# Optimization experiments

Measured on AMD Instinct MI355X. Metric: run time of the kernel, lower is better.

Reference implementation:

```python
import jax, jax.numpy as jnp
import numpy as np

E, T, H, I, K = 16, 2048, 1024, 512, 2  # experts, tokens, hidden, intermediate, top_k


def setup_inputs() -> dict:
    key = jax.random.key(0)
    k1, k2, k3, k4, k5 = jax.random.split(key, 5)
    hidden_states = jax.random.normal(k1, (T, H), dtype=jnp.float32)
    topk_weights = jax.random.uniform(k2, (T, K), dtype=jnp.float32)
    topk_indices = jax.random.randint(k3, (T, K), 0, E, dtype=jnp.int32)
    # learned expert params, viewed per expert as in _view_experts_weight()
    gate_up_proj = jax.random.normal(k4, (E, H, 2 * I), dtype=jnp.float32) * 0.02
    down_proj = jax.random.normal(k5, (E, I, H), dtype=jnp.float32) * 0.02
    return {
        "hidden_states": hidden_states,
        "topk_weights": topk_weights,
        "topk_indices": topk_indices,
        "gate_up_proj": gate_up_proj,
        "down_proj": down_proj,
    }


def reference(hidden_states, topk_weights, topk_indices, gate_up_proj, down_proj):
    """MoE experts: per-expert gate_up GEMM -> silu-gate -> down GEMM,
    combined with top-k routing weights (index_add over tokens in the original).

    Equivalent dense formulation: combine[e, t] = sum_k topk_weights[t, k] * [topk_indices[t, k] == e];
    out = sum_e expert_e(hidden_states) * combine[e][:, None]. Tokens not routed to e get
    weight 0, matching the original gather/scatter-add exactly (including duplicate
    expert ids within a token, which accumulate).
    """
    num_experts = gate_up_proj.shape[0]
    one_hot = jax.nn.one_hot(topk_indices, num_experts, dtype=topk_weights.dtype)  # [T, K, E]
    combine = jnp.einsum("tk,tke->et", topk_weights, one_hot)  # [E, T]

    def body(acc, xs):
        w_gu, w_d, w = xs  # [H, 2I], [I, H], [T]
        gate_up = hidden_states @ w_gu  # [T, 2I]
        gate, up = jnp.split(gate_up, 2, axis=-1)
        expert_out = (jax.nn.silu(gate) * up) @ w_d  # [T, H]
        return acc + expert_out * w[:, None], None

    init = jnp.zeros_like(hidden_states)
    out, _ = jax.lax.scan(body, init, (gate_up_proj, down_proj, combine))
    return out.astype(hidden_states.dtype)
```

## Files before the change

### kernel.cpp

```cpp
#include <hip/hip_runtime.h>

#define E_ 16
#define T_ 2048
#define H_ 1024
#define I_ 512
#define K_ 2
#define NPAIR (T_*K_)

typedef __bf16 bf16x8 __attribute__((ext_vector_type(8)));
typedef float  f32x4  __attribute__((ext_vector_type(4)));

static __device__ __forceinline__ unsigned short f2bf(float f) {
    __bf16 h = (__bf16)f;
    return __builtin_bit_cast(unsigned short, h);
}

__global__ __launch_bounds__(256) void route_kernel(
    const float* __restrict__ tw, const int* __restrict__ ti,
    int* __restrict__ offs, int* __restrict__ pair_ts, float* __restrict__ pair_w)
{
    __shared__ unsigned short hist[256][E_];
    __shared__ int ebase[E_];
    const int tid = threadIdx.x;

    int e_loc[16];
    unsigned short h[E_];
    for (int e = 0; e < E_; ++e) h[e] = 0;
    for (int i = 0; i < 16; ++i) {
        int p = tid * 16 + i;
        int e = ti[p];
        e_loc[i] = e;
        h[e]++;
    }
    for (int e = 0; e < E_; ++e) hist[tid][e] = h[e];
    __syncthreads();

    if (tid < E_) {
        int e = tid, run = 0;
        for (int t = 0; t < 256; ++t) {
            unsigned short c = hist[t][e];
            hist[t][e] = (unsigned short)run;
            run += c;
        }
        ebase[e] = run;
    }
    __syncthreads();
    if (tid == 0) {
        int run = 0;
        for (int e = 0; e < E_; ++e) { int c = ebase[e]; offs[e] = run; ebase[e] = run; run += c; }
        offs[E_] = run;
    }
    __syncthreads();

    int cur[E_];
    for (int e = 0; e < E_; ++e) cur[e] = ebase[e] + hist[tid][e];
    for (int i = 0; i < 16; ++i) {
        int p = tid * 16 + i;
        int e = e_loc[i];
        int pos = cur[e]++;
        pair_ts[pos] = p;
        pair_w[pos]  = tw[p];
    }
}

__global__ __launch_bounds__(256) void gather_kernel(
    const float* __restrict__ X, const int* __restrict__ pair_ts,
    unsigned short* __restrict__ Ag)
{
    const int q = blockIdx.x;
    const int t = pair_ts[q] >> 1;
    const int c = threadIdx.x * 4;
    const float4 x = *(const float4*)&X[(size_t)t * H_ + c];
    ushort4 b; b.x = f2bf(x.x); b.y = f2bf(x.y); b.z = f2bf(x.z); b.w = f2bf(x.w);
    *(ushort4*)&Ag[(size_t)q * H_ + c] = b;
}

#define LDK 70

__global__ __launch_bounds__(256) void gemm1_kernel(
    const unsigned short* __restrict__ Ag, const float* __restrict__ W1,
    const int* __restrict__ offs, unsigned short* __restrict__ act)
{
    const int e    = blockIdx.z;
    const int rbeg = offs[e], rend = offs[e + 1];
    const int ne   = rend - rbeg;
    const int row0 = blockIdx.y * 256;
    if (row0 >= ne) return;
    const int c0 = blockIdx.x * 32;

    __shared__ unsigned short As[256][LDK];
    __shared__ unsigned short Bs[64][LDK];

    const int tid = threadIdx.x;
    const float* __restrict__ W1e = W1 + (size_t)e * H_ * (2 * I_);

    const int ar = tid >> 3;
    const int ac = (tid & 7) * 8;
    int aq[8];
    for (int i = 0; i < 8; ++i) {
        int q = rbeg + row0 + ar + i * 32;
        aq[i] = q < rend ? q : rend - 1;
    }

    const int bn   = tid & 63;
    const int bks  = tid >> 6;
    const int bcol = (bn < 32) ? (c0 + bn) : (I_ + c0 + (bn - 32));

    f32x4 acc[4][4];
    for (int m = 0; m < 4; ++m)
        for (int n = 0; n < 4; ++n)
            acc[m][n] = f32x4{0.f, 0.f, 0.f, 0.f};

    const int lane = tid & 63;
    const int w    = tid >> 6;
    const int lrow = lane & 15;
    const int lk   = lane >> 4;

    for (int kt = 0; kt < H_ / 64; ++kt) {
        const int kb = kt * 64;
        #pragma unroll
        for (int i = 0; i < 8; ++i) {
            const uint4 x = *(const uint4*)&Ag[(size_t)aq[i] * H_ + kb + ac];
            *(uint4*)&As[ar + i * 32][ac] = x;
        }
        {
            float v[16];
            #pragma unroll
            for (int i = 0; i < 16; ++i)
                v[i] = W1e[(size_t)(kb + bks * 16 + i) * (2 * I_) + bcol];
            #pragma unroll
            for (int i = 0; i < 16; i += 4) {
                ushort4 p;
                p.x = f2bf(v[i]); p.y = f2bf(v[i+1]); p.z = f2bf(v[i+2]); p.w = f2bf(v[i+3]);
                *(ushort4*)&Bs[bn][bks * 16 + i] = p;
            }
        }
        __syncthreads();
        #pragma unroll
        for (int kk = 0; kk < 64; kk += 32) {
            bf16x8 af[4], bfr[4];
            #pragma unroll
            for (int m = 0; m < 4; ++m)
                af[m] = *(const bf16x8*)&As[w * 64 + m * 16 + lrow][kk + lk * 8];
            #pragma unroll
            for (int n = 0; n < 4; ++n)
                bfr[n] = *(const bf16x8*)&Bs[n * 16 + lrow][kk + lk * 8];
            #pragma unroll
            for (int m = 0; m < 4; ++m)
                #pragma unroll
                for (int n = 0; n < 4; ++n)
                    acc[m][n] = __builtin_amdgcn_mfma_f32_16x16x32_bf16(af[m], bfr[n], acc[m][n], 0, 0, 0);
        }
        __syncthreads();
    }

    for (int m = 0; m < 4; ++m) {
        for (int reg = 0; reg < 4; ++reg) {
            int rloc = w * 64 + m * 16 + lk * 4 + reg;
            if (row0 + rloc < ne) {
                int q = rbeg + row0 + rloc;
                #pragma unroll
                for (int fn = 0; fn < 2; ++fn) {
                    float g = acc[m][fn][reg];
                    float u = acc[m][fn + 2][reg];
                    float a = g / (1.f + __expf(-g)) * u;
                    act[(size_t)q * I_ + c0 + fn * 16 + lrow] = f2bf(a);
                }
            }
        }
    }
}

__global__ __launch_bounds__(256) void gemm2_kernel(
    const unsigned short* __restrict__ act, const float* __restrict__ W2,
    const int* __restrict__ offs, const int* __restrict__ pair_ts,
    const float* __restrict__ pair_w, float* __restrict__ out)
{
    const int e    = blockIdx.z;
    const int rbeg = offs[e], rend = offs[e + 1];
    const int ne   = rend - rbeg;
    const int row0 = blockIdx.y * 256;
    if (row0 >= ne) return;
    const int c0 = blockIdx.x * 64;

    __shared__ unsigned short As[256][LDK];
    __shared__ unsigned short Bs[64][LDK];

    const int tid = threadIdx.x;
    const float* __restrict__ W2e = W2 + (size_t)e * I_ * H_;

    const int ar = tid >> 3;
    const int ac = (tid & 7) * 8;
    int aq[8];
    for (int i = 0; i < 8; ++i) {
        int q = rbeg + row0 + ar + i * 32;
        aq[i] = q < rend ? q : rend - 1;
    }

    const int bn  = tid & 63;
    const int bks = tid >> 6;

    f32x4 acc[4][4];
    for (int m = 0; m < 4; ++m)
        for (int n = 0; n < 4; ++n)
            acc[m][n] = f32x4{0.f, 0.f, 0.f, 0.f};

    const int lane = tid & 63;
    const int w    = tid >> 6;
    const int lrow = lane & 15;
    const int lk   = lane >> 4;

    for (int kt = 0; kt < I_ / 64; ++kt) {
        const int kb = kt * 64;
        #pragma unroll
        for (int i = 0; i < 8; ++i) {
            const uint4 x = *(const uint4*)&act[(size_t)aq[i] * I_ + kb + ac];
            *(uint4*)&As[ar + i * 32][ac] = x;
        }
        {
            float v[16];
            #pragma unroll
            for (int i = 0; i < 16; ++i)
                v[i] = W2e[(size_t)(kb + bks * 16 + i) * H_ + c0 + bn];
            #pragma unroll
            for (int i = 0; i < 16; i += 4) {
                ushort4 p;
                p.x = f2bf(v[i]); p.y = f2bf(v[i+1]); p.z = f2bf(v[i+2]); p.w = f2bf(v[i+3]);
                *(ushort4*)&Bs[bn][bks * 16 + i] = p;
            }
        }
        __syncthreads();
        #pragma unroll
        for (int kk = 0; kk < 64; kk += 32) {
            bf16x8 af[4], bfr[4];
            #pragma unroll
            for (int m = 0; m < 4; ++m)
                af[m] = *(const bf16x8*)&As[w * 64 + m * 16 + lrow][kk + lk * 8];
            #pragma unroll
            for (int n = 0; n < 4; ++n)
                bfr[n] = *(const bf16x8*)&Bs[n * 16 + lrow][kk + lk * 8];
            #pragma unroll
            for (int m = 0; m < 4; ++m)
                #pragma unroll
                for (int n = 0; n < 4; ++n)
                    acc[m][n] = __builtin_amdgcn_mfma_f32_16x16x32_bf16(af[m], bfr[n], acc[m][n], 0, 0, 0);
        }
        __syncthreads();
    }

    for (int m = 0; m < 4; ++m) {
        for (int reg = 0; reg < 4; ++reg) {
            int rloc = w * 64 + m * 16 + lk * 4 + reg;
            if (row0 + rloc < ne) {
                int q   = rbeg + row0 + rloc;
                int t   = pair_ts[q] >> 1;
                float wt = pair_w[q];
                #pragma unroll
                for (int fn = 0; fn < 4; ++fn) {
                    int cg = c0 + fn * 16 + lrow;
                    atomicAdd(&out[(size_t)t * H_ + cg], wt * acc[m][fn][reg]);
                }
            }
        }
    }
}

extern "C" void kernel_launch(void* const* d_in, const int* in_sizes, int n_in,
                              void* d_out, int out_size, void* d_ws, size_t ws_size,
                              hipStream_t stream)
{
    const float* X  = (const float*)d_in[0];
    const float* tw = (const float*)d_in[1];
    const int*   ti = (const int*)d_in[2];
    const float* W1 = (const float*)d_in[3];
    const float* W2 = (const float*)d_in[4];
    float* out = (float*)d_out;

    char* ws = (char*)d_ws;
    int*   offs    = (int*)(ws);
    int*   pair_ts = (int*)(ws + 256);
    float* pair_w  = (float*)(ws + 256 + NPAIR * 4);
    unsigned short* Ag  = (unsigned short*)(ws + (1u << 16));
    unsigned short* act = (unsigned short*)(ws + (1u << 16) + (size_t)NPAIR * H_ * 2);

    hipMemsetAsync(d_out, 0, (size_t)out_size * sizeof(float), stream);

    route_kernel<<<1, 256, 0, stream>>>(tw, ti, offs, pair_ts, pair_w);

    gather_kernel<<<NPAIR, 256, 0, stream>>>(X, pair_ts, Ag);

    gemm1_kernel<<<dim3(I_ / 32, NPAIR / 256, E_), 256, 0, stream>>>(Ag, W1, offs, act);

    gemm2_kernel<<<dim3(H_ / 64, NPAIR / 256, E_), 256, 0, stream>>>(act, W2, offs, pair_ts, pair_w, out);
}
```

Baseline: 97.11 us.

## Double-buffer GEMM tiles with direct global-to-LDS loads, XOR swizzle, 8 waves

Both expert GEMM kernels now double-buffer their LDS tiles, prefetching the next K-slice while MFMAs run on the current one. The activation tile is loaded with global_load_lds straight into shared memory. Padded LDS rows are replaced by an XOR swizzle to avoid bank conflicts. Blocks grow to 512 threads as a 4x2 wave grid so each wave holds fewer accumulators. LDS use doubles, which may lower occupancy, and the swizzled layout must stay consistent between the load and read paths.

Result: slower. 110.1 us (+13.4%).

```diff
diff --git a/kernel.cpp b/kernel.cpp
--- a/kernel.cpp
+++ b/kernel.cpp
@@ -4,8 +4,7 @@
 #define T_ 2048
 #define H_ 1024
 #define I_ 512
-#define K_ 2
-#define NPAIR (T_*K_)
+#define NPAIR 4096
 
 typedef __bf16 bf16x8 __attribute__((ext_vector_type(8)));
 typedef float  f32x4  __attribute__((ext_vector_type(4)));
@@ -13,6 +12,20 @@
 static __device__ __forceinline__ unsigned short f2bf(float f) {
     __bf16 h = (__bf16)f;
     return __builtin_bit_cast(unsigned short, h);
+}
+
+static __device__ __forceinline__ uint4 pack8(const float* v) {
+    union { unsigned short us[8]; uint4 u; } r;
+    #pragma unroll
+    for (int i = 0; i < 8; ++i) r.us[i] = f2bf(v[i]);
+    return r.u;
+}
+
+static __device__ __forceinline__ void gl_lds16(const void* g, void* l) {
+    __builtin_amdgcn_global_load_lds(
+        (const __attribute__((address_space(1))) unsigned int*)g,
+        (__attribute__((address_space(3))) unsigned int*)l,
+        16, 0, 0);
 }
 
 __global__ __launch_bounds__(256) void route_kernel(
@@ -75,9 +88,7 @@
     *(ushort4*)&Ag[(size_t)q * H_ + c] = b;
 }
 
-#define LDK 70
-
-__global__ __launch_bounds__(256) void gemm1_kernel(
+__global__ __launch_bounds__(512) void gemm1_kernel(
     const unsigned short* __restrict__ Ag, const float* __restrict__ W1,
     const int* __restrict__ offs, unsigned short* __restrict__ act)
 {
@@ -88,90 +99,100 @@
     if (row0 >= ne) return;
     const int c0 = blockIdx.x * 32;
 
-    __shared__ unsigned short As[256][LDK];
-    __shared__ unsigned short Bs[64][LDK];
-
-    const int tid = threadIdx.x;
-    const float* __restrict__ W1e = W1 + (size_t)e * H_ * (2 * I_);
-
-    const int ar = tid >> 3;
-    const int ac = (tid & 7) * 8;
-    int aq[8];
-    for (int i = 0; i < 8; ++i) {
-        int q = rbeg + row0 + ar + i * 32;
-        aq[i] = q < rend ? q : rend - 1;
-    }
-
-    const int bn   = tid & 63;
-    const int bks  = tid >> 6;
-    const int bcol = (bn < 32) ? (c0 + bn) : (I_ + c0 + (bn - 32));
-
-    f32x4 acc[4][4];
-    for (int m = 0; m < 4; ++m)
-        for (int n = 0; n < 4; ++n)
-            acc[m][n] = f32x4{0.f, 0.f, 0.f, 0.f};
-
+    __shared__ unsigned short As[2][256][64];
+    __shared__ unsigned short Bs[2][64][64];
+
+    const int tid  = threadIdx.x;
     const int lane = tid & 63;
     const int w    = tid >> 6;
+    const int wm   = w >> 1;
+    const int wn   = w & 1;
     const int lrow = lane & 15;
     const int lk   = lane >> 4;
 
+    const float* __restrict__ W1e = W1 + (size_t)e * (H_ * 2 * I_);
+
+    const int r8 = lane >> 3, gr = lane & 7;
+    const unsigned short* asrc[4];
+    for (int i = 0; i < 4; ++i) {
+        int rl = w * 32 + i * 8 + r8;
+        int q  = rbeg + row0 + rl;
+        if (q > rend - 1) q = rend - 1;
+        asrc[i] = Ag + (size_t)q * H_ + ((gr ^ r8) * 8);
+    }
+
+    const int bn    = lane;
+    const int bcol  = ((bn >> 4) & 1) * I_ + c0 + (bn >> 5) * 16 + (bn & 15);
+    const int bwoff = ((w ^ (bn & 7)) * 8);
+    const float* __restrict__ bsrc = W1e + (size_t)(w * 8) * (2 * I_) + bcol;
+
+    f32x4 acc[4][2];
+    for (int m = 0; m < 4; ++m)
+        for (int n = 0; n < 2; ++n)
+            acc[m][n] = f32x4{0.f, 0.f, 0.f, 0.f};
+
+    #pragma unroll
+    for (int i = 0; i < 4; ++i) gl_lds16(asrc[i], &As[0][w * 32 + i * 8][0]);
+    {
+        float bv[8];
+        #pragma unroll
+        for (int i = 0; i < 8; ++i) bv[i] = bsrc[(size_t)i * (2 * I_)];
+        *(uint4*)&Bs[0][bn][bwoff] = pack8(bv);
+    }
+    __syncthreads();
+
+    int cur = 0;
     for (int kt = 0; kt < H_ / 64; ++kt) {
-        const int kb = kt * 64;
-        #pragma unroll
-        for (int i = 0; i < 8; ++i) {
-            const uint4 x = *(const uint4*)&Ag[(size_t)aq[i] * H_ + kb + ac];
-            *(uint4*)&As[ar + i * 32][ac] = x;
-        }
-        {
-            float v[16];
-            #pragma unroll
-            for (int i = 0; i < 16; ++i)
-                v[i] = W1e[(size_t)(kb + bks * 16 + i) * (2 * I_) + bcol];
-            #pragma unroll
-            for (int i = 0; i < 16; i += 4) {
-                ushort4 p;
-                p.x = f2bf(v[i]); p.y = f2bf(v[i+1]); p.z = f2bf(v[i+2]); p.w = f2bf(v[i+3]);
-                *(ushort4*)&Bs[bn][bks * 16 + i] = p;
-            }
-        }
-        __syncthreads();
+        const int nxt = cur ^ 1;
+        const bool more = (kt + 1) < H_ / 64;
+        float bv[8];
+        if (more) {
+            const int kb = (kt + 1) * 64;
+            #pragma unroll
+            for (int i = 0; i < 4; ++i) gl_lds16(asrc[i] + kb, &As[nxt][w * 32 + i * 8][0]);
+            #pragma unroll
+            for (int i = 0; i < 8; ++i) bv[i] = bsrc[(size_t)(kb + i) * (2 * I_)];
+        }
         #pragma unroll
         for (int kk = 0; kk < 64; kk += 32) {
-            bf16x8 af[4], bfr[4];
-            #pragma unroll
-            for (int m = 0; m < 4; ++m)
-                af[m] = *(const bf16x8*)&As[w * 64 + m * 16 + lrow][kk + lk * 8];
-            #pragma unroll
-            for (int n = 0; n < 4; ++n)
-                bfr[n] = *(const bf16x8*)&Bs[n * 16 + lrow][kk + lk * 8];
+            const int j0 = kk >> 3;
+            bf16x8 af[4], bfr[2];
+            #pragma unroll
+            for (int m = 0; m < 4; ++m) {
+                int row = wm * 64 + m * 16 + lrow;
+                af[m] = *(const bf16x8*)&As[cur][row][((j0 + lk) ^ (row & 7)) * 8];
+            }
+            #pragma unroll
+            for (int n = 0; n < 2; ++n) {
+                int col = wn * 32 + n * 16 + lrow;
+                bfr[n] = *(const bf16x8*)&Bs[cur][col][((j0 + lk) ^ (col & 7)) * 8];
+            }
             #pragma unroll
             for (int m = 0; m < 4; ++m)
                 #pragma unroll
-                for (int n = 0; n < 4; ++n)
+                for (int n = 0; n < 2; ++n)
                     acc[m][n] = __builtin_amdgcn_mfma_f32_16x16x32_bf16(af[m], bfr[n], acc[m][n], 0, 0, 0);
         }
+        if (more) *(uint4*)&Bs[nxt][bn][bwoff] = pack8(bv);
         __syncthreads();
+        cur = nxt;
     }
 
     for (int m = 0; m < 4; ++m) {
+        #pragma unroll
         for (int reg = 0; reg < 4; ++reg) {
-            int rloc = w * 64 + m * 16 + lk * 4 + reg;
+            int rloc = wm * 64 + m * 16 + lk * 4 + reg;
             if (row0 + rloc < ne) {
                 int q = rbeg + row0 + rloc;
-                #pragma unroll
-                for (int fn = 0; fn < 2; ++fn) {
-                    float g = acc[m][fn][reg];
-                    float u = acc[m][fn + 2][reg];
-                    float a = g / (1.f + __expf(-g)) * u;
-                    act[(size_t)q * I_ + c0 + fn * 16 + lrow] = f2bf(a);
-                }
-            }
-        }
-    }
-}
-
-__global__ __launch_bounds__(256) void gemm2_kernel(
+                float g = acc[m][0][reg], u = acc[m][1][reg];
+                float a = g / (1.f + __expf(-g)) * u;
+                act[(size_t)q * I_ + c0 + wn * 16 + lrow] = f2bf(a);
+            }
+        }
+    }
+}
+
+__global__ __launch_bounds__(512) void gemm2_kernel(
     const unsigned short* __restrict__ act, const float* __restrict__ W2,
     const int* __restrict__ offs, const int* __restrict__ pair_ts,
     const float* __restrict__ pair_w, float* __restrict__ out)
@@ -183,82 +204,96 @@
     if (row0 >= ne) return;
     const int c0 = blockIdx.x * 64;
 
-    __shared__ unsigned short As[256][LDK];
-    __shared__ unsigned short Bs[64][LDK];
-
-    const int tid = threadIdx.x;
-    const float* __restrict__ W2e = W2 + (size_t)e * I_ * H_;
-
-    const int ar = tid >> 3;
-    const int ac = (tid & 7) * 8;
-    int aq[8];
-    for (int i = 0; i < 8; ++i) {
-        int q = rbeg + row0 + ar + i * 32;
-        aq[i] = q < rend ? q : rend - 1;
-    }
-
-    const int bn  = tid & 63;
-    const int bks = tid >> 6;
-
-    f32x4 acc[4][4];
-    for (int m = 0; m < 4; ++m)
-        for (int n = 0; n < 4; ++n)
-            acc[m][n] = f32x4{0.f, 0.f, 0.f, 0.f};
-
+    __shared__ unsigned short As[2][256][64];
+    __shared__ unsigned short Bs[2][64][64];
+
+    const int tid  = threadIdx.x;
     const int lane = tid & 63;
     const int w    = tid >> 6;
+    const int wm   = w >> 1;
+    const int wn   = w & 1;
     const int lrow = lane & 15;
     const int lk   = lane >> 4;
 
+    const float* __restrict__ W2e = W2 + (size_t)e * (I_ * H_);
+
+    const int r8 = lane >> 3, gr = lane & 7;
+    const unsigned short* asrc[4];
+    for (int i = 0; i < 4; ++i) {
+        int rl = w * 32 + i * 8 + r8;
+        int q  = rbeg + row0 + rl;
+        if (q > rend - 1) q = rend - 1;
+        asrc[i] = act + (size_t)q * I_ + ((gr ^ r8) * 8);
+    }
+
+    const int bn    = lane;
+    const int bwoff = ((w ^ (bn & 7)) * 8);
+    const float* __restrict__ bsrc = W2e + (size_t)(w * 8) * H_ + c0 + bn;
+
+    f32x4 acc[4][2];
+    for (int m = 0; m < 4; ++m)
+        for (int n = 0; n < 2; ++n)
+            acc[m][n] = f32x4{0.f, 0.f, 0.f, 0.f};
+
+    #pragma unroll
+    for (int i = 0; i < 4; ++i) gl_lds16(asrc[i], &As[0][w * 32 + i * 8][0]);
+    {
+        float bv[8];
+        #pragma unroll
+        for (int i = 0; i < 8; ++i) bv[i] = bsrc[(size_t)i * H_];
+        *(uint4*)&Bs[0][bn][bwoff] = pack8(bv);
+    }
+    __syncthreads();
+
+    int cur = 0;
     for (int kt = 0; kt < I_ / 64; ++kt) {
-        const int kb = kt * 64;
-        #pragma unroll
-        for (int i = 0; i < 8; ++i) {
-            const uint4 x = *(const uint4*)&act[(size_t)aq[i] * I_ + kb + ac];
-            *(uint4*)&As[ar + i * 32][ac] = x;
-        }
-        {
-            float v[16];
-            #pragma unroll
-            for (int i = 0; i < 16; ++i)
-                v[i] = W2e[(size_t)(kb + bks * 16 + i) * H_ + c0 + bn];
-            #pragma unroll
-            for (int i = 0; i < 16; i += 4) {
-                ushort4 p;
-                p.x = f2bf(v[i]); p.y = f2bf(v[i+1]); p.z = f2bf(v[i+2]); p.w = f2bf(v[i+3]);
-                *(ushort4*)&Bs[bn][bks * 16 + i] = p;
-            }
-        }
-        __syncthreads();
+        const int nxt = cur ^ 1;
+        const bool more = (kt + 1) < I_ / 64;
+        float bv[8];
+        if (more) {
+            const int kb = (kt + 1) * 64;
+            #pragma unroll
+            for (int i = 0; i < 4; ++i) gl_lds16(asrc[i] + kb, &As[nxt][w * 32 + i * 8][0]);
+            #pragma unroll
+            for (int i = 0; i < 8; ++i) bv[i] = bsrc[(size_t)(kb + i) * H_];
+        }
         #pragma unroll
         for (int kk = 0; kk < 64; kk += 32) {
-            bf16x8 af[4], bfr[4];
-            #pragma unroll
-            for (int m = 0; m < 4; ++m)
-                af[m] = *(const bf16x8*)&As[w * 64 + m * 16 + lrow][kk + lk * 8];
-            #pragma unroll
-            for (int n = 0; n < 4; ++n)
-                bfr[n] = *(const bf16x8*)&Bs[n * 16 + lrow][kk + lk * 8];
+            const int j0 = kk >> 3;
+            bf16x8 af[4], bfr[2];
+            #pragma unroll
+            for (int m = 0; m < 4; ++m) {
+                int row = wm * 64 + m * 16 + lrow;
+                af[m] = *(const bf16x8*)&As[cur][row][((j0 + lk) ^ (row & 7)) * 8];
+            }
+            #pragma unroll
+            for (int n = 0; n < 2; ++n) {
+                int col = wn * 32 + n * 16 + lrow;
+                bfr[n] = *(const bf16x8*)&Bs[cur][col][((j0 + lk) ^ (col & 7)) * 8];
+            }
             #pragma unroll
             for (int m = 0; m < 4; ++m)
                 #pragma unroll
-                for (int n = 0; n < 4; ++n)
+                for (int n = 0; n < 2; ++n)
                     acc[m][n] = __builtin_amdgcn_mfma_f32_16x16x32_bf16(af[m], bfr[n], acc[m][n], 0, 0, 0);
         }
+        if (more) *(uint4*)&Bs[nxt][bn][bwoff] = pack8(bv);
         __syncthreads();
+        cur = nxt;
     }
 
     for (int m = 0; m < 4; ++m) {
+        #pragma unroll
         for (int reg = 0; reg < 4; ++reg) {
-            int rloc = w * 64 + m * 16 + lk * 4 + reg;
+            int rloc = wm * 64 + m * 16 + lk * 4 + reg;
             if (row0 + rloc < ne) {
                 int q   = rbeg + row0 + rloc;
                 int t   = pair_ts[q] >> 1;
                 float wt = pair_w[q];
                 #pragma unroll
-                for (int fn = 0; fn < 4; ++fn) {
-                    int cg = c0 + fn * 16 + lrow;
-                    atomicAdd(&out[(size_t)t * H_ + cg], wt * acc[m][fn][reg]);
+                for (int n = 0; n < 2; ++n) {
+                    int cg = c0 + wn * 32 + n * 16 + lrow;
+                    atomicAdd(&out[(size_t)t * H_ + cg], wt * acc[m][n][reg]);
                 }
             }
         }
@@ -289,7 +324,7 @@
 
     gather_kernel<<<NPAIR, 256, 0, stream>>>(X, pair_ts, Ag);
 
-    gemm1_kernel<<<dim3(I_ / 32, NPAIR / 256, E_), 256, 0, stream>>>(Ag, W1, offs, act);
-
-    gemm2_kernel<<<dim3(H_ / 64, NPAIR / 256, E_), 256, 0, stream>>>(act, W2, offs, pair_ts, pair_w, out);
-}
+    gemm1_kernel<<<dim3(I_ / 32, NPAIR / 256, E_), 512, 0, stream>>>(Ag, W1, offs, act);
+
+    gemm2_kernel<<<dim3(H_ / 64, NPAIR / 256, E_), 512, 0, stream>>>(act, W2, offs, pair_ts, pair_w, out);
+}
```
